# Performance work log

Hardware: AMD Instinct MI355X
Metric: run time of the kernel (lower is better)

The kernel has to match this reference:

```python
import jax, jax.numpy as jnp
import numpy as np

INPUT_DIM = 1024
EMBED_DIM = 1024
NUM_HEADS = 16
HEAD_DIM = EMBED_DIM // NUM_HEADS


def _xavier_uniform(key, shape):
    fan_in, fan_out = shape[1], shape[0]
    limit = float(np.sqrt(6.0 / (fan_in + fan_out)))
    return jax.random.uniform(key, shape, jnp.float32, -limit, limit)


def setup_inputs() -> dict:
    key = jax.random.key(0)
    kx, kqkv, ko = jax.random.split(key, 3)
    return {
        "x": jax.random.normal(kx, (2, 2048, INPUT_DIM), jnp.float32),
        "qkv_w": _xavier_uniform(kqkv, (3 * EMBED_DIM, INPUT_DIM)),
        "qkv_b": jnp.zeros((3 * EMBED_DIM,), jnp.float32),
        "o_w": _xavier_uniform(ko, (EMBED_DIM, INPUT_DIM)),
        "o_b": jnp.zeros((EMBED_DIM,), jnp.float32),
    }


def reference(x, qkv_w, qkv_b, o_w, o_b):
    B, S, _ = x.shape
    scale = HEAD_DIM ** -0.5
    # fused QKV projection: [B,S,3E]
    qkv = jnp.einsum('bsd,ed->bse', x, qkv_w) + qkv_b
    # [B,S,H,3Dh] -> [B,H,S,3Dh], then split into q,k,v
    qkv = qkv.reshape(B, S, NUM_HEADS, 3 * HEAD_DIM).transpose(0, 2, 1, 3)
    q, k, v = jnp.split(qkv, 3, axis=-1)
    # scaled dot-product attention
    scores = jnp.einsum('bhqd,bhkd->bhqk', q, k) * scale
    attn = jax.nn.softmax(scores, axis=-1)
    values = jnp.einsum('bhqk,bhkd->bhqd', attn, v)
    # [B,H,S,Dh] -> [B,S,E]
    values = values.transpose(0, 2, 1, 3).reshape(B, S, EMBED_DIM)
    return jnp.einsum('bse,oe->bso', values, o_w) + o_b
```

## Files before the change

### kernel.cpp

```cpp
#include <hip/hip_runtime.h>
#include <hip/hip_bf16.h>

typedef __bf16  bf16x8 __attribute__((ext_vector_type(8)));
typedef __bf16  bf16x4 __attribute__((ext_vector_type(4)));
typedef float   f32x4  __attribute__((ext_vector_type(4)));

#define LOG2E 1.44269504088896340736f

__device__ __forceinline__ void async_copy16(const void* g, void* l) {
  __builtin_amdgcn_global_load_lds(
      (const __attribute__((address_space(1))) unsigned int*)g,
      (__attribute__((address_space(3))) unsigned int*)l, 16, 0, 0);
}

#define C0 524288
#define C1 393216
#define C2 384
#define C3 131072
#define C4 128
#define CTOT (C0 + C1 + C2 + C3 + C4)
__global__ void convert_all(const void* __restrict__ x,  const void* __restrict__ qw,
                            const void* __restrict__ qb, const void* __restrict__ ow,
                            const void* __restrict__ ob,
                            __bf16* __restrict__ cx,  __bf16* __restrict__ cqw,
                            __bf16* __restrict__ cqb, __bf16* __restrict__ cow,
                            __bf16* __restrict__ cob, int* __restrict__ flag) {
  __shared__ int cnt;
  if (threadIdx.x == 0) cnt = 0;
  __syncthreads();
  unsigned int w = ((const unsigned int*)qw)[threadIdx.x];
  if (w & 0x4000u) atomicAdd(&cnt, 1);
  __syncthreads();
  const int f = (cnt > 16) ? 1 : 0;
  if (threadIdx.x == 0) *flag = f;

  int i = blockIdx.x * blockDim.x + threadIdx.x;
  const int stride = gridDim.x * blockDim.x;
  for (; i < CTOT; i += stride) {
    const void* s; __bf16* d; int off;
    if      (i < C0)                { s = x;  d = cx;  off = i; }
    else if (i < C0 + C1)           { s = qw; d = cqw; off = i - C0; }
    else if (i < C0 + C1 + C2)      { s = qb; d = cqb; off = i - C0 - C1; }
    else if (i < C0 + C1 + C2 + C3) { s = ow; d = cow; off = i - C0 - C1 - C2; }
    else                            { s = ob; d = cob; off = i - C0 - C1 - C2 - C3; }
    if (f) {
      const f32x4* sp = (const f32x4*)s;
      f32x4 a = sp[2 * off], b = sp[2 * off + 1];
      bf16x8 o;
      o[0] = (__bf16)a[0]; o[1] = (__bf16)a[1]; o[2] = (__bf16)a[2]; o[3] = (__bf16)a[3];
      o[4] = (__bf16)b[0]; o[5] = (__bf16)b[1]; o[6] = (__bf16)b[2]; o[7] = (__bf16)b[3];
      *(bf16x8*)&d[8 * off] = o;
    } else {
      *(bf16x8*)&d[8 * off] = ((const bf16x8*)s)[off];
    }
  }
}

template<int BN>
__global__ __launch_bounds__(256) void gemm_nt_bias(
    const __bf16* __restrict__ A,
    const __bf16* __restrict__ Bt,
    const __bf16* __restrict__ bias,
    __bf16* __restrict__ Cb,
    float* __restrict__ Cf,
    __bf16* __restrict__ vt,
    const int* __restrict__ flag,
    int M, int N, int K)
{
  constexpr int NI  = BN / 32;
  constexpr int NIB = BN / 32;
  __shared__ __align__(16) __bf16 As[128 * 64];
  __shared__ __align__(16) __bf16 Bs[BN * 64];

  const int tid  = threadIdx.x;
  const int lane = tid & 63;
  const int wave = tid >> 6;
  const int qd   = lane >> 4;
  const int ln   = lane & 15;
  const int m0 = blockIdx.y * 128;
  const int n0 = blockIdx.x * BN;
  const int wm = (wave >> 1) * 64;
  const int wn = (wave & 1) * (16 * NI);

  f32x4 acc[4][NI] = {};

  for (int kt = 0; kt < K; kt += 64) {
#pragma unroll
    for (int i = 0; i < 4; ++i) {
      int s = wave * 256 + i * 64 + lane;
      int r = s >> 3;
      int c = (s & 7) ^ (r & 7);
      async_copy16(A + (size_t)(m0 + r) * K + kt + c * 8, &As[(wave * 256 + i * 64) * 8]);
    }
#pragma unroll
    for (int i = 0; i < NIB; ++i) {
      int s = wave * (64 * NIB) + i * 64 + lane;
      int r = s >> 3;
      int c = (s & 7) ^ (r & 7);
      async_copy16(Bt + (size_t)(n0 + r) * K + kt + c * 8,
                   &Bs[(wave * (64 * NIB) + i * 64) * 8]);
    }
    __syncthreads();

#pragma unroll
    for (int kk = 0; kk < 2; ++kk) {
      bf16x8 af[4], bfr[NI];
#pragma unroll
      for (int t = 0; t < 4; ++t) {
        int ra = wm + t * 16 + ln;
        af[t] = *(const bf16x8*)&As[ra * 64 + (((kk * 4 + qd) ^ (ra & 7)) * 8)];
      }
#pragma unroll
      for (int t = 0; t < NI; ++t) {
        int rb = wn + t * 16 + ln;
        bfr[t] = *(const bf16x8*)&Bs[rb * 64 + (((kk * 4 + qd) ^ (rb & 7)) * 8)];
      }
#pragma unroll
      for (int mi = 0; mi < 4; ++mi)
#pragma unroll
        for (int ni = 0; ni < NI; ++ni)
          acc[mi][ni] = __builtin_amdgcn_mfma_f32_16x16x32_bf16(af[mi], bfr[ni], acc[mi][ni], 0, 0, 0);
    }
    __syncthreads();
  }

  const bool f32out = (Cf != nullptr) && (*flag != 0);
#pragma unroll
  for (int ni = 0; ni < NI; ++ni) {
    int cb0 = n0 + wn + ni * 16;
    int col = cb0 + ln;
    float bv = (float)bias[col];
    int grp = cb0 % 192;
    if (vt != nullptr && grp >= 128) {
      int hh = cb0 / 192;
      int d  = grp - 128 + ln;
#pragma unroll
      for (int mi = 0; mi < 4; ++mi) {
        int row0 = m0 + wm + mi * 16 + qd * 4;
        int bb = row0 >> 11, ss = row0 & 2047;
        bf16x4 w;
#pragma unroll
        for (int r = 0; r < 4; ++r) w[r] = (__bf16)(acc[mi][ni][r] + bv);
        *(bf16x4*)&vt[(((size_t)(bb * 16 + hh) * 64 + d) * 2048 + ss)] = w;
      }
    } else {
#pragma unroll
      for (int mi = 0; mi < 4; ++mi) {
#pragma unroll
        for (int r = 0; r < 4; ++r) {
          int row = m0 + wm + mi * 16 + qd * 4 + r;
          float v = acc[mi][ni][r] + bv;
          if (f32out) Cf[(size_t)row * N + col] = v;
          else        Cb[(size_t)row * N + col] = (__bf16)v;
        }
      }
    }
  }
}

#define PST 72
__global__ __launch_bounds__(256) void attn_flash(
    const __bf16* __restrict__ qkv,
    const __bf16* __restrict__ vt,
    __bf16* __restrict__ vals)
{
  __shared__ __align__(16) unsigned char smem[102400];
  __bf16* Ksb = (__bf16*)smem;
  __bf16* VTb = (__bf16*)(smem + 32768);
  __bf16* Ps  = (__bf16*)(smem + 65536);

  const int tid  = threadIdx.x;
  const int lane = tid & 63;
  const int wave = tid >> 6;
  const int sh   = wave >> 1;
  const int wq   = wave & 1;
  const int qd   = lane >> 4;
  const int ln   = lane & 15;
  const int b  = blockIdx.y >> 4;
  const int h  = blockIdx.y & 15;
  const int q0 = blockIdx.x * 128;
  const __bf16* base = qkv + (size_t)b * 2048 * 3072 + h * 192;
  const __bf16* vbase = vt + (size_t)(b * 16 + h) * 64 * 2048;
  const int khalf = sh * 1024;

  bf16x8 qfr[4][2];
#pragma unroll
  for (int nt = 0; nt < 4; ++nt)
#pragma unroll
    for (int ks = 0; ks < 2; ++ks)
      qfr[nt][ks] = *(const bf16x8*)&base[(size_t)(q0 + wq * 64 + nt * 16 + ln) * 3072
                                          + ks * 32 + qd * 8];

  const float kScale = 0.125f * LOG2E;
  __bf16* P = Ps + wave * (64 * PST);

  f32x4 oaccT[4][4] = {};
  float lpart[4] = {0.f, 0.f, 0.f, 0.f};

#pragma unroll
  for (int i = 0; i < 4; ++i) {
    int s = wq * 256 + i * 64 + lane;
    int r = s >> 3;
    int c = (s & 7) ^ (r & 7);
    async_copy16(base + (size_t)(khalf + r) * 3072 + 64 + c * 8,
                 &Ksb[sh * 4096 + (wq * 256 + i * 64) * 8]);
    async_copy16(vbase + (size_t)r * 2048 + khalf + c * 8,
                 &VTb[sh * 4096 + (wq * 256 + i * 64) * 8]);
  }

  for (int it = 0; it < 16; ++it) {
    const int buf  = (it & 1) * 8192;
    const int nbuf = ((it + 1) & 1) * 8192;
    __syncthreads();

    {
      const int ktn = khalf + (((it + 1) & 15) << 6);
#pragma unroll
      for (int i = 0; i < 4; ++i) {
        int s = wq * 256 + i * 64 + lane;
        int r = s >> 3;
        int c = (s & 7) ^ (r & 7);
        async_copy16(base + (size_t)(ktn + r) * 3072 + 64 + c * 8,
                     &Ksb[nbuf + sh * 4096 + (wq * 256 + i * 64) * 8]);
        async_copy16(vbase + (size_t)r * 2048 + ktn + c * 8,
                     &VTb[nbuf + sh * 4096 + (wq * 256 + i * 64) * 8]);
      }
    }

    f32x4 sacc[4][4] = {};
#pragma unroll
    for (int ks = 0; ks < 2; ++ks) {
      bf16x8 kfr[4];
#pragma unroll
      for (int mi = 0; mi < 4; ++mi) {
        int row = mi * 16 + ln;
        kfr[mi] = *(const bf16x8*)&Ksb[buf + sh * 4096 + row * 64
                                       + (((ks * 4 + qd) ^ (row & 7)) * 8)];
      }
#pragma unroll
      for (int nt = 0; nt < 4; ++nt)
#pragma unroll
        for (int mi = 0; mi < 4; ++mi)
          sacc[nt][mi] = __builtin_amdgcn_mfma_f32_16x16x32_bf16(kfr[mi], qfr[nt][ks], sacc[nt][mi], 0, 0, 0);
    }

#pragma unroll
    for (int nt = 0; nt < 4; ++nt) {
      float rs = 0.f;
#pragma unroll
      for (int mi = 0; mi < 4; ++mi) {
        float pv[4];
#pragma unroll
        for (int r = 0; r < 4; ++r) {
          pv[r] = __builtin_exp2f(sacc[nt][mi][r] * kScale);
          rs += pv[r];
        }
        bf16x4 w;
        w[0] = (__bf16)pv[0]; w[1] = (__bf16)pv[1];
        w[2] = (__bf16)pv[2]; w[3] = (__bf16)pv[3];
        *(bf16x4*)&P[(nt * 16 + ln) * PST + mi * 16 + qd * 4] = w;
      }
      lpart[nt] += rs;
    }

    asm volatile("s_waitcnt lgkmcnt(0)" ::: "memory");

#pragma unroll
    for (int ks = 0; ks < 2; ++ks) {
      bf16x8 vfr[4], pfr[4];
#pragma unroll
      for (int md = 0; md < 4; ++md) {
        int row = md * 16 + ln;
        vfr[md] = *(const bf16x8*)&VTb[buf + sh * 4096 + row * 64
                                       + (((ks * 4 + qd) ^ (row & 7)) * 8)];
      }
#pragma unroll
      for (int nt = 0; nt < 4; ++nt)
        pfr[nt] = *(const bf16x8*)&P[(nt * 16 + ln) * PST + ks * 32 + qd * 8];
#pragma unroll
      for (int nt = 0; nt < 4; ++nt)
#pragma unroll
        for (int md = 0; md < 4; ++md)
          oaccT[nt][md] = __builtin_amdgcn_mfma_f32_16x16x32_bf16(vfr[md], pfr[nt], oaccT[nt][md], 0, 0, 0);
    }
  }

  float lw[4];
#pragma unroll
  for (int nt = 0; nt < 4; ++nt) {
    float l = lpart[nt];
    l += __shfl_xor(l, 16);
    l += __shfl_xor(l, 32);
    lw[nt] = l;
  }
  __syncthreads();

  float* Sc = (float*)smem;
  float* Ls = (float*)(smem + 32768);

  if (sh == 0) {
#pragma unroll
    for (int nt = 0; nt < 4; ++nt) {
#pragma unroll
      for (int md = 0; md < 4; ++md)
        *(f32x4*)&Sc[((size_t)(wq * 64 + nt * 16 + ln)) * 64 + md * 16 + qd * 4] = oaccT[nt][md];
      if (qd == 0) Ls[wq * 64 + nt * 16 + ln] = lw[nt];
    }
  }
  __syncthreads();
  if (sh == 1) {
#pragma unroll
    for (int nt = 0; nt < 4; ++nt) {
      float il = 1.0f / (lw[nt] + Ls[wq * 64 + nt * 16 + ln]);
      int q = q0 + wq * 64 + nt * 16 + ln;
      __bf16* o = vals + ((size_t)b * 2048 + q) * 1024 + h * 64;
#pragma unroll
      for (int md = 0; md < 4; ++md) {
        f32x4 part = *(const f32x4*)&Sc[((size_t)(wq * 64 + nt * 16 + ln)) * 64 + md * 16 + qd * 4];
        bf16x4 w;
#pragma unroll
        for (int r = 0; r < 4; ++r)
          w[r] = (__bf16)((oaccT[nt][md][r] + part[r]) * il);
        *(bf16x4*)&o[md * 16 + qd * 4] = w;
      }
    }
  }
}

extern "C" void kernel_launch(void* const* d_in, const int* in_sizes, int n_in,
                              void* d_out, int out_size, void* d_ws, size_t ws_size,
                              hipStream_t stream) {
  __bf16* ws    = (__bf16*)d_ws;
  __bf16* qkv   = ws;
  __bf16* vals  = qkv   + (size_t)4096 * 3072;
  __bf16* cx    = vals  + (size_t)4096 * 1024;
  __bf16* cqkvw = cx    + (size_t)4096 * 1024;
  __bf16* cow   = cqkvw + (size_t)3072 * 1024;
  __bf16* cqkvb = cow   + (size_t)1024 * 1024;
  __bf16* cob   = cqkvb + 4096;
  int*    flag  = (int*)(cob + 4096);
  __bf16* vT    = (__bf16*)(flag + 64);

  dim3 blk(256);

  convert_all<<<1024, 256, 0, stream>>>(d_in[0], d_in[1], d_in[2], d_in[3], d_in[4],
                                        cx, cqkvw, cqkvb, cow, cob, flag);

  gemm_nt_bias<128><<<dim3(3072 / 128, 4096 / 128), blk, 0, stream>>>(
      cx, cqkvw, cqkvb, qkv, nullptr, vT, flag, 4096, 3072, 1024);

  attn_flash<<<dim3(2048 / 128, 32), blk, 0, stream>>>(qkv, vT, vals);

  gemm_nt_bias<64><<<dim3(1024 / 64, 4096 / 128), blk, 0, stream>>>(
      vals, cow, cob, (__bf16*)d_out, (float*)d_out, nullptr, flag, 4096, 1024, 1024);
}
```

Baseline: 223.6 us.

## Drop K/V double buffering in attention to fit two blocks per CU

Replaces the double-buffered K and V^T LDS tiles with single buffers, shrinking shared memory from 100KB to 68KB, and adds launch_bounds(256,2) so two workgroups can be resident per CU. Each iteration now issues its async loads and then waits on a second barrier before computing, so the prefetch overlap inside a block is lost. The bet is that the extra resident block hides load latency better than in-block pipelining; the register cap from the launch bound may also cause spills.

```diff
diff --git a/kernel.cpp b/kernel.cpp
--- a/kernel.cpp
+++ b/kernel.cpp
@@ -159,15 +159,15 @@
 }
 
 #define PST 72
-__global__ __launch_bounds__(256) void attn_flash(
+__global__ __launch_bounds__(256, 2) void attn_flash(
     const __bf16* __restrict__ qkv,
     const __bf16* __restrict__ vt,
     __bf16* __restrict__ vals)
 {
-  __shared__ __align__(16) unsigned char smem[102400];
-  __bf16* Ksb = (__bf16*)smem;
-  __bf16* VTb = (__bf16*)(smem + 32768);
-  __bf16* Ps  = (__bf16*)(smem + 65536);
+  __shared__ __align__(16) unsigned char smem[69632];
+  __bf16* Ks  = (__bf16*)smem;
+  __bf16* VTs = (__bf16*)(smem + 16384);
+  __bf16* Ps  = (__bf16*)(smem + 32768);
 
   const int tid  = threadIdx.x;
   const int lane = tid & 63;
@@ -197,35 +197,21 @@
   f32x4 oaccT[4][4] = {};
   float lpart[4] = {0.f, 0.f, 0.f, 0.f};
 
-#pragma unroll
-  for (int i = 0; i < 4; ++i) {
-    int s = wq * 256 + i * 64 + lane;
-    int r = s >> 3;
-    int c = (s & 7) ^ (r & 7);
-    async_copy16(base + (size_t)(khalf + r) * 3072 + 64 + c * 8,
-                 &Ksb[sh * 4096 + (wq * 256 + i * 64) * 8]);
-    async_copy16(vbase + (size_t)r * 2048 + khalf + c * 8,
-                 &VTb[sh * 4096 + (wq * 256 + i * 64) * 8]);
-  }
-
   for (int it = 0; it < 16; ++it) {
-    const int buf  = (it & 1) * 8192;
-    const int nbuf = ((it + 1) & 1) * 8192;
+    const int kt = khalf + it * 64;
     __syncthreads();
 
-    {
-      const int ktn = khalf + (((it + 1) & 15) << 6);
-#pragma unroll
-      for (int i = 0; i < 4; ++i) {
-        int s = wq * 256 + i * 64 + lane;
-        int r = s >> 3;
-        int c = (s & 7) ^ (r & 7);
-        async_copy16(base + (size_t)(ktn + r) * 3072 + 64 + c * 8,
-                     &Ksb[nbuf + sh * 4096 + (wq * 256 + i * 64) * 8]);
-        async_copy16(vbase + (size_t)r * 2048 + ktn + c * 8,
-                     &VTb[nbuf + sh * 4096 + (wq * 256 + i * 64) * 8]);
-      }
-    }
+#pragma unroll
+    for (int i = 0; i < 4; ++i) {
+      int s  = wq * 256 + i * 64 + lane;
+      int r  = s >> 3;
+      int c  = (s & 7) ^ (r & 7);
+      async_copy16(base + (size_t)(kt + r) * 3072 + 64 + c * 8,
+                   &Ks[sh * 4096 + (wq * 256 + i * 64) * 8]);
+      async_copy16(vbase + (size_t)r * 2048 + kt + c * 8,
+                   &VTs[sh * 4096 + (wq * 256 + i * 64) * 8]);
+    }
+    __syncthreads();
 
     f32x4 sacc[4][4] = {};
 #pragma unroll
@@ -234,8 +220,7 @@
 #pragma unroll
       for (int mi = 0; mi < 4; ++mi) {
         int row = mi * 16 + ln;
-        kfr[mi] = *(const bf16x8*)&Ksb[buf + sh * 4096 + row * 64
-                                       + (((ks * 4 + qd) ^ (row & 7)) * 8)];
+        kfr[mi] = *(const bf16x8*)&Ks[sh * 4096 + row * 64 + (((ks * 4 + qd) ^ (row & 7)) * 8)];
       }
 #pragma unroll
       for (int nt = 0; nt < 4; ++nt)
@@ -271,8 +256,7 @@
 #pragma unroll
       for (int md = 0; md < 4; ++md) {
         int row = md * 16 + ln;
-        vfr[md] = *(const bf16x8*)&VTb[buf + sh * 4096 + row * 64
-                                       + (((ks * 4 + qd) ^ (row & 7)) * 8)];
+        vfr[md] = *(const bf16x8*)&VTs[sh * 4096 + row * 64 + (((ks * 4 + qd) ^ (row & 7)) * 8)];
       }
 #pragma unroll
       for (int nt = 0; nt < 4; ++nt)
```

After: 196.7 us. 1.14x faster.
